# Kernel tuning notes

Hardware: AMD Instinct MI355X
Metric: run time of the kernel (lower is better)

## Reference

```python
import jax, jax.numpy as jnp
import numpy as np

FEATURE_SIZE = 1_000_000
FIELD_SIZE = 39
DIM = 16
BATCH = 8192
CROSS = FIELD_SIZE * (FIELD_SIZE - 1) // 2  # 741


def _pair_index():
    # [[i, j] for i in range(F-1) for j in range(i+1, F)] -> [CROSS, 2]
    idx = [[i, j] for i in range(FIELD_SIZE - 1) for j in range(i + 1, FIELD_SIZE)]
    return jnp.asarray(np.array(idx, dtype=np.int32))


def setup_inputs() -> dict:
    key = jax.random.key(0)
    k1, k2, k3, k4 = jax.random.split(key, 4)
    inputs = jax.random.randint(k1, (BATCH, FIELD_SIZE), 0, FEATURE_SIZE, dtype=jnp.int32)
    embedding_weights = jax.random.normal(k2, (FEATURE_SIZE, DIM), dtype=jnp.float32) * 0.05
    field_weights = jax.random.normal(k3, (CROSS, 1), dtype=jnp.float32) * 0.1
    linear_weights = jax.random.normal(k4, (FEATURE_SIZE,), dtype=jnp.float32) * 0.05
    bias_weight = jnp.zeros((), dtype=jnp.float32)
    return {
        "inputs": inputs,
        "embedding_weights": embedding_weights,
        "field_weights": field_weights,
        "linear_weights": linear_weights,
        "bias_weight": bias_weight,
    }


def reference(inputs, embedding_weights, field_weights, linear_weights, bias_weight):
    pair_idx = _pair_index()  # [CROSS, 2]

    # first order: sum of linear weights over fields -> [B, 1]
    first_order = jnp.sum(linear_weights[inputs], axis=1, keepdims=True)
    bias = jnp.ones_like(first_order) * bias_weight

    # gather each field's embedding once, then index the pairs (same math as
    # the double gather in the original, avoids re-gathering the big table)
    field_emb = embedding_weights[inputs]            # [B, F, D]
    e_i = field_emb[:, pair_idx[:, 0], :]            # [B, CROSS, D]
    e_j = field_emb[:, pair_idx[:, 1], :]            # [B, CROSS, D]
    second_items = jnp.sum(e_i * e_j, axis=-1)       # [B, CROSS]
    second_order = second_items @ field_weights      # [B, 1]

    return bias + first_order + second_order
```

## Files before the change

kernel.cpp:

```cpp
#include <hip/hip_runtime.h>
#include <utility>

#define FIELD 39
#define TILE  13
#define DIM   16
#define BATCH 8192
#define EPAD  42

constexpr int widx(int i, int j) { return i*(FIELD-1) - i*(i-1)/2 + (j-i-1); }
constexpr int ceil4(int x) { return (x+3) & ~3; }
constexpr int OFF_ROW  = 16;
constexpr int OFF_TILE = TILE * OFF_ROW;
constexpr int diag_rowstart(int II) {
    int s = 0; for (int m = 0; m < II; ++m) s += ceil4(TILE-1-m); return s;
}
constexpr int DIAG_TILE = diag_rowstart(TILE);
constexpr int off_base(int t) { return t * OFF_TILE; }
constexpr int diag_base(int A) { return 3*OFF_TILE + A*DIAG_TILE; }
constexpr int WTOT = 3*OFF_TILE + 3*DIAG_TILE;

struct WMap { int v[WTOT]; };
constexpr WMap make_map() {
    WMap m{};
    for (int i = 0; i < WTOT; ++i) m.v[i] = -1;
    const int AB[3][2] = {{0,1},{0,2},{1,2}};
    for (int t = 0; t < 3; ++t)
        for (int II = 0; II < TILE; ++II)
            for (int c = 0; c < TILE; ++c)
                m.v[off_base(t) + II*OFF_ROW + c] = widx(AB[t][0]*TILE+II, AB[t][1]*TILE+c);
    for (int A = 0; A < 3; ++A)
        for (int II = 0; II < TILE-1; ++II)
            for (int k = 0; k < TILE-1-II; ++k)
                m.v[diag_base(A) + diag_rowstart(II) + k] = widx(A*TILE+II, A*TILE+II+1+k);
    return m;
}
__device__ constexpr WMap g_map = make_map();

__device__ __forceinline__ float4 ld4(const float* lds, int ofs) {
    return *reinterpret_cast<const float4*>(lds + ofs);
}
template <int EB>
__device__ __forceinline__ float fma4(float4 w, const float (&e)[EPAD], float s) {
    s = fmaf(w.x, e[EB+0], s); s = fmaf(w.y, e[EB+1], s);
    s = fmaf(w.z, e[EB+2], s); s = fmaf(w.w, e[EB+3], s);
    return s;
}
template <int RBASE, int EBASE, size_t... Qs>
__device__ __forceinline__ float row_q(const float* lds, const float (&e)[EPAD],
                                       std::index_sequence<Qs...>) {
    float s = 0.f;
    ((s = fma4<EBASE + 4*(int)Qs>(ld4(lds, RBASE + 4*(int)Qs), e, s)), ...);
    return s;
}
template <int T, int A, int B, size_t... IIs>
__device__ __forceinline__ void block_off(const float* lds, const float (&e)[EPAD],
                                          float (&acc)[4], std::index_sequence<IIs...>) {
    ((acc[IIs & 3] = fmaf(e[A*TILE + (int)IIs],
         row_q<off_base(T) + (int)IIs*OFF_ROW, B*TILE>(lds, e, std::make_index_sequence<4>{}),
         acc[IIs & 3])), ...);
}
template <int A, size_t... IIs>
__device__ __forceinline__ void block_diag(const float* lds, const float (&e)[EPAD],
                                           float (&acc)[4], std::index_sequence<IIs...>) {
    ((acc[IIs & 3] = fmaf(e[A*TILE + (int)IIs],
         row_q<diag_base(A) + diag_rowstart((int)IIs), A*TILE + (int)IIs + 1>(
             lds, e, std::make_index_sequence<(size_t)(ceil4(TILE-1-(int)IIs)/4)>{}),
         acc[IIs & 3])), ...);
}
template <size_t... Fs>
__device__ __forceinline__ void gather_all(const int* __restrict__ rowIdx,
                                           const float* __restrict__ emb,
                                           int d, float (&e)[EPAD],
                                           std::index_sequence<Fs...>) {
    int idx[FIELD];
    ((idx[Fs] = rowIdx[Fs]), ...);
    ((e[Fs] = emb[(size_t)idx[Fs] * DIM + d]), ...);
}

__global__ __launch_bounds__(256, 2) void fwfm_kernel(
    const int*   __restrict__ inputs,
    const float* __restrict__ emb,
    const float* __restrict__ fw,
    const float* __restrict__ lw,
    const float* __restrict__ bias,
    float*       __restrict__ out)
{
    __shared__ __align__(16) float wlds[WTOT];

    const int tid  = threadIdx.x;
    const int lane = tid & 63;
    const int wave = tid >> 6;
    const int d    = lane & 15;
    const int rloc = lane >> 4;
    const int row  = blockIdx.x * 16 + wave * 4 + rloc;

    const int* rowIdx = inputs + row * FIELD;

    float e[EPAD];
    gather_all(rowIdx, emb, d, e, std::make_index_sequence<FIELD>{});
    e[39] = 0.f; e[40] = 0.f; e[41] = 0.f;

    for (int s = tid; s < WTOT; s += 256) {
        int m = g_map.v[s];
        wlds[s] = (m >= 0) ? fw[m] : 0.f;
    }
    __syncthreads();

    float fo = lw[rowIdx[d]] + lw[rowIdx[d + 16]];
    if (d < 7) fo += lw[rowIdx[d + 32]];

    float acc[4] = {0.f, 0.f, 0.f, 0.f};
    const auto seqT = std::make_index_sequence<TILE>{};
    block_off<0, 0, 1>(wlds, e, acc, seqT);
    block_off<1, 0, 2>(wlds, e, acc, seqT);
    block_off<2, 1, 2>(wlds, e, acc, seqT);
    block_diag<0>(wlds, e, acc, seqT);
    block_diag<1>(wlds, e, acc, seqT);
    block_diag<2>(wlds, e, acc, seqT);
    float so = (acc[0] + acc[1]) + (acc[2] + acc[3]);

    float tot = fo + so;
    tot += __shfl_xor(tot, 1, 64);
    tot += __shfl_xor(tot, 2, 64);
    tot += __shfl_xor(tot, 4, 64);
    tot += __shfl_xor(tot, 8, 64);

    if (d == 0) out[row] = tot + bias[0];
}

extern "C" void kernel_launch(void* const* d_in, const int* in_sizes, int n_in,
                              void* d_out, int out_size, void* d_ws, size_t ws_size,
                              hipStream_t stream) {
    const int*   inputs = (const int*)  d_in[0];
    const float* emb    = (const float*)d_in[1];
    const float* fw     = (const float*)d_in[2];
    const float* lw     = (const float*)d_in[3];
    const float* bias   = (const float*)d_in[4];
    float*       out    = (float*)      d_out;

    dim3 grid(BATCH / 16);
    fwfm_kernel<<<grid, 256, 0, stream>>>(inputs, emb, fw, lw, bias, out);
}
```

Baseline: 108.3 us.

## Stage embedding rows in LDS via coalesced float4 gathers

Indices for the block's 16 rows are first staged into LDS. Each 64-byte embedding row is then gathered cooperatively with float4 loads and stored in LDS, and each thread reads its per-dimension scalars from there. This replaces 39 scalar 4-byte gathers per thread with wide vector loads that issue fewer memory transactions. In exchange it uses about 41 KB of LDS per block and adds an extra barrier, which could lower occupancy.

```diff
diff --git a/kernel.cpp b/kernel.cpp
--- a/kernel.cpp
+++ b/kernel.cpp
@@ -6,6 +6,9 @@
 #define DIM   16
 #define BATCH 8192
 #define EPAD  42
+#define RPB   16
+#define ROWF  (FIELD * DIM)
+#define CHUNKS (RPB * FIELD * 4)
 
 constexpr int widx(int i, int j) { return i*(FIELD-1) - i*(i-1)/2 + (j-i-1); }
 constexpr int ceil4(int x) { return (x+3) & ~3; }
@@ -68,13 +71,9 @@
          acc[IIs & 3])), ...);
 }
 template <size_t... Fs>
-__device__ __forceinline__ void gather_all(const int* __restrict__ rowIdx,
-                                           const float* __restrict__ emb,
-                                           int d, float (&e)[EPAD],
-                                           std::index_sequence<Fs...>) {
-    int idx[FIELD];
-    ((idx[Fs] = rowIdx[Fs]), ...);
-    ((e[Fs] = emb[(size_t)idx[Fs] * DIM + d]), ...);
+__device__ __forceinline__ void eread(const float* __restrict__ elds_row, int d,
+                                      float (&e)[EPAD], std::index_sequence<Fs...>) {
+    ((e[Fs] = elds_row[(int)Fs * DIM + d]), ...);
 }
 
 __global__ __launch_bounds__(256, 2) void fwfm_kernel(
@@ -85,29 +84,47 @@
     const float* __restrict__ bias,
     float*       __restrict__ out)
 {
+    __shared__ __align__(16) float elds[RPB * ROWF];
+    __shared__ int   ilds[RPB * FIELD];
     __shared__ __align__(16) float wlds[WTOT];
 
-    const int tid  = threadIdx.x;
-    const int lane = tid & 63;
-    const int wave = tid >> 6;
-    const int d    = lane & 15;
-    const int rloc = lane >> 4;
-    const int row  = blockIdx.x * 16 + wave * 4 + rloc;
+    const int tid = threadIdx.x;
 
-    const int* rowIdx = inputs + row * FIELD;
-
-    float e[EPAD];
-    gather_all(rowIdx, emb, d, e, std::make_index_sequence<FIELD>{});
-    e[39] = 0.f; e[40] = 0.f; e[41] = 0.f;
-
+    const int* ibase = inputs + blockIdx.x * (RPB * FIELD);
+    for (int s = tid; s < RPB * FIELD; s += 256) ilds[s] = ibase[s];
     for (int s = tid; s < WTOT; s += 256) {
         int m = g_map.v[s];
         wlds[s] = (m >= 0) ? fw[m] : 0.f;
     }
     __syncthreads();
 
-    float fo = lw[rowIdx[d]] + lw[rowIdx[d + 16]];
-    if (d < 7) fo += lw[rowIdx[d + 32]];
+    float4 v[10];
+    #pragma unroll
+    for (int k = 0; k < 10; ++k) {
+        int c = tid + (k << 8);
+        c = (c < CHUNKS) ? c : 0;
+        v[k] = *(const float4*)(emb + (size_t)ilds[c >> 2] * DIM + ((c & 3) << 2));
+    }
+    #pragma unroll
+    for (int k = 0; k < 10; ++k) {
+        int c = tid + (k << 8);
+        if (c < CHUNKS) *(float4*)(elds + (c << 2)) = v[k];
+    }
+    __syncthreads();
+
+    const int lane = tid & 63;
+    const int wave = tid >> 6;
+    const int d    = lane & 15;
+    const int rloc = lane >> 4;
+    const int row  = wave * 4 + rloc;
+
+    const int* ri = ilds + row * FIELD;
+    float l0 = lw[ri[d]], l1 = lw[ri[d + 16]];
+    float l2 = (d < 7) ? lw[ri[d + 32]] : 0.f;
+
+    float e[EPAD];
+    eread(elds + row * ROWF, d, e, std::make_index_sequence<FIELD>{});
+    e[39] = 0.f; e[40] = 0.f; e[41] = 0.f;
 
     float acc[4] = {0.f, 0.f, 0.f, 0.f};
     const auto seqT = std::make_index_sequence<TILE>{};
@@ -119,13 +136,13 @@
     block_diag<2>(wlds, e, acc, seqT);
     float so = (acc[0] + acc[1]) + (acc[2] + acc[3]);
 
-    float tot = fo + so;
+    float tot = so + (l0 + l1 + l2);
     tot += __shfl_xor(tot, 1, 64);
     tot += __shfl_xor(tot, 2, 64);
     tot += __shfl_xor(tot, 4, 64);
     tot += __shfl_xor(tot, 8, 64);
 
-    if (d == 0) out[row] = tot + bias[0];
+    if (d == 0) out[blockIdx.x * RPB + row] = tot + bias[0];
 }
 
 extern "C" void kernel_launch(void* const* d_in, const int* in_sizes, int n_in,
@@ -138,6 +155,6 @@
     const float* bias   = (const float*)d_in[4];
     float*       out    = (float*)      d_out;
 
-    dim3 grid(BATCH / 16);
+    dim3 grid(BATCH / RPB);
     fwfm_kernel<<<grid, 256, 0, stream>>>(inputs, emb, fw, lw, bias, out);
 }
```

Result: slower. 110.5 us (+2.0%).

## Flatten pair-weight layout, issue linear-weight loads early, use nontemporal gathers

Applied to the files above, without the earlier changes.

Replaces the 3x3 tiled weight layout with a flat per-row triangular LDS layout padded to multiples of four. The linear-weight loads now reuse the index registers and are issued right after the embedding gathers, before the barrier, so their latency overlaps the LDS weight fill. Embedding gathers use nontemporal loads to avoid polluting the cache with single-use table rows. The flat layout changes the padding overhead (more padded FMAs for odd row lengths), and nontemporal loads may behave differently for the randomly accessed table.

```diff
diff --git a/kernel.cpp b/kernel.cpp
--- a/kernel.cpp
+++ b/kernel.cpp
@@ -2,36 +2,25 @@
 #include <utility>
 
 #define FIELD 39
-#define TILE  13
 #define DIM   16
 #define BATCH 8192
 #define EPAD  42
 
 constexpr int widx(int i, int j) { return i*(FIELD-1) - i*(i-1)/2 + (j-i-1); }
 constexpr int ceil4(int x) { return (x+3) & ~3; }
-constexpr int OFF_ROW  = 16;
-constexpr int OFF_TILE = TILE * OFF_ROW;
-constexpr int diag_rowstart(int II) {
-    int s = 0; for (int m = 0; m < II; ++m) s += ceil4(TILE-1-m); return s;
+constexpr int rowlen(int i) { return ceil4(FIELD - 1 - i); }
+constexpr int rowstart(int i) {
+    int s = 0; for (int m = 0; m < i; ++m) s += rowlen(m); return s;
 }
-constexpr int DIAG_TILE = diag_rowstart(TILE);
-constexpr int off_base(int t) { return t * OFF_TILE; }
-constexpr int diag_base(int A) { return 3*OFF_TILE + A*DIAG_TILE; }
-constexpr int WTOT = 3*OFF_TILE + 3*DIAG_TILE;
+constexpr int WTOT = rowstart(FIELD - 1);
 
 struct WMap { int v[WTOT]; };
 constexpr WMap make_map() {
     WMap m{};
     for (int i = 0; i < WTOT; ++i) m.v[i] = -1;
-    const int AB[3][2] = {{0,1},{0,2},{1,2}};
-    for (int t = 0; t < 3; ++t)
-        for (int II = 0; II < TILE; ++II)
-            for (int c = 0; c < TILE; ++c)
-                m.v[off_base(t) + II*OFF_ROW + c] = widx(AB[t][0]*TILE+II, AB[t][1]*TILE+c);
-    for (int A = 0; A < 3; ++A)
-        for (int II = 0; II < TILE-1; ++II)
-            for (int k = 0; k < TILE-1-II; ++k)
-                m.v[diag_base(A) + diag_rowstart(II) + k] = widx(A*TILE+II, A*TILE+II+1+k);
+    for (int i = 0; i < FIELD - 1; ++i)
+        for (int k = 0; k < FIELD - 1 - i; ++k)
+            m.v[rowstart(i) + k] = widx(i, i + 1 + k);
     return m;
 }
 __device__ constexpr WMap g_map = make_map();
@@ -45,36 +34,33 @@
     s = fmaf(w.z, e[EB+2], s); s = fmaf(w.w, e[EB+3], s);
     return s;
 }
-template <int RBASE, int EBASE, size_t... Qs>
-__device__ __forceinline__ float row_q(const float* lds, const float (&e)[EPAD],
-                                       std::index_sequence<Qs...>) {
+template <int I, size_t... Qs>
+__device__ __forceinline__ float row_sum(const float* lds, const float (&e)[EPAD],
+                                         std::index_sequence<Qs...>) {
     float s = 0.f;
-    ((s = fma4<EBASE + 4*(int)Qs>(ld4(lds, RBASE + 4*(int)Qs), e, s)), ...);
+    ((s = fma4<I + 1 + 4*(int)Qs>(ld4(lds, rowstart(I) + 4*(int)Qs), e, s)), ...);
     return s;
 }
-template <int T, int A, int B, size_t... IIs>
-__device__ __forceinline__ void block_off(const float* lds, const float (&e)[EPAD],
-                                          float (&acc)[4], std::index_sequence<IIs...>) {
-    ((acc[IIs & 3] = fmaf(e[A*TILE + (int)IIs],
-         row_q<off_base(T) + (int)IIs*OFF_ROW, B*TILE>(lds, e, std::make_index_sequence<4>{}),
-         acc[IIs & 3])), ...);
-}
-template <int A, size_t... IIs>
-__device__ __forceinline__ void block_diag(const float* lds, const float (&e)[EPAD],
-                                           float (&acc)[4], std::index_sequence<IIs...>) {
-    ((acc[IIs & 3] = fmaf(e[A*TILE + (int)IIs],
-         row_q<diag_base(A) + diag_rowstart((int)IIs), A*TILE + (int)IIs + 1>(
-             lds, e, std::make_index_sequence<(size_t)(ceil4(TILE-1-(int)IIs)/4)>{}),
-         acc[IIs & 3])), ...);
+template <size_t... Is>
+__device__ __forceinline__ float pair_sum(const float* lds, const float (&e)[EPAD],
+                                          std::index_sequence<Is...>) {
+    float acc[4] = {0.f, 0.f, 0.f, 0.f};
+    ((acc[Is & 3] = fmaf(e[Is],
+         row_sum<(int)Is>(lds, e, std::make_index_sequence<(size_t)(rowlen((int)Is)/4)>{}),
+         acc[Is & 3])), ...);
+    return (acc[0] + acc[1]) + (acc[2] + acc[3]);
 }
 template <size_t... Fs>
-__device__ __forceinline__ void gather_all(const int* __restrict__ rowIdx,
+__device__ __forceinline__ void gather_all(const int (&idx)[FIELD],
                                            const float* __restrict__ emb,
                                            int d, float (&e)[EPAD],
                                            std::index_sequence<Fs...>) {
-    int idx[FIELD];
+    ((e[Fs] = __builtin_nontemporal_load(emb + (size_t)idx[Fs] * DIM + d)), ...);
+}
+template <size_t... Fs>
+__device__ __forceinline__ void load_idx(const int* __restrict__ rowIdx,
+                                         int (&idx)[FIELD], std::index_sequence<Fs...>) {
     ((idx[Fs] = rowIdx[Fs]), ...);
-    ((e[Fs] = emb[(size_t)idx[Fs] * DIM + d]), ...);
 }
 
 __global__ __launch_bounds__(256, 2) void fwfm_kernel(
@@ -96,9 +82,14 @@
 
     const int* rowIdx = inputs + row * FIELD;
 
+    int idx[FIELD];
+    load_idx(rowIdx, idx, std::make_index_sequence<FIELD>{});
     float e[EPAD];
-    gather_all(rowIdx, emb, d, e, std::make_index_sequence<FIELD>{});
+    gather_all(idx, emb, d, e, std::make_index_sequence<FIELD>{});
     e[39] = 0.f; e[40] = 0.f; e[41] = 0.f;
+
+    float l0 = lw[idx[d]], l1 = lw[idx[d + 16]];
+    float l2 = (d < 7) ? lw[idx[d + 32]] : 0.f;
 
     for (int s = tid; s < WTOT; s += 256) {
         int m = g_map.v[s];
@@ -106,20 +97,9 @@
     }
     __syncthreads();
 
-    float fo = lw[rowIdx[d]] + lw[rowIdx[d + 16]];
-    if (d < 7) fo += lw[rowIdx[d + 32]];
+    float so = pair_sum(wlds, e, std::make_index_sequence<FIELD - 1>{});
 
-    float acc[4] = {0.f, 0.f, 0.f, 0.f};
-    const auto seqT = std::make_index_sequence<TILE>{};
-    block_off<0, 0, 1>(wlds, e, acc, seqT);
-    block_off<1, 0, 2>(wlds, e, acc, seqT);
-    block_off<2, 1, 2>(wlds, e, acc, seqT);
-    block_diag<0>(wlds, e, acc, seqT);
-    block_diag<1>(wlds, e, acc, seqT);
-    block_diag<2>(wlds, e, acc, seqT);
-    float so = (acc[0] + acc[1]) + (acc[2] + acc[3]);
-
-    float tot = fo + so;
+    float tot = so + (l0 + l1 + l2);
     tot += __shfl_xor(tot, 1, 64);
     tot += __shfl_xor(tot, 2, 64);
     tot += __shfl_xor(tot, 4, 64);
```

Result: slower. 118.8 us (+9.7%).
